# Kernel optimization log

Hardware: AMD Instinct MI355X
Metric: run time of the kernel (lower is better)

The kernel has to match this reference:

```python
import jax, jax.numpy as jnp
import numpy as np

# init kwargs (constants)
P = 1            # chamfer_distance_p
WEIGHT = 1.0
XYZ_UNIT = 0.1


def setup_inputs() -> dict:
    key = jax.random.key(0)
    k1, k2 = jax.random.split(key)
    B, N, M, D = 16, 4096, 4096, 3
    pred = jax.random.normal(k1, (B, N, D), dtype=jnp.float32)
    gt = jax.random.normal(k2, (B, M, D), dtype=jnp.float32)
    return {"pred": pred, "gt": gt}


def _chamfer(x, y, p):
    x2 = jnp.sum(x * x, axis=-1)                       # [B, N]
    y2 = jnp.sum(y * y, axis=-1)                       # [B, M]
    xy = jnp.einsum('bnd,bmd->bnm', x, y)              # [B, N, M]
    sq = jnp.maximum(x2[:, :, None] + y2[:, None, :] - 2.0 * xy, 0.0)
    dist = jnp.sqrt(sq)                                # torch.norm(x-y, dim=3)
    if p != 1:
        dist = dist ** p
    x_loss = jnp.mean(jnp.min(dist, axis=2), axis=1)   # [B]
    y_loss = jnp.mean(jnp.min(dist, axis=1), axis=1)   # [B]
    return jnp.mean(x_loss + y_loss)                   # scalar (reduce=True)


def reference(pred, gt):
    # HelperPointLoss.forward with reduce_over_batch=True, loss_name='chamfer_distance'
    loss = _chamfer(pred, gt, P)
    # info['helper_loss'] = loss (detached); info['helper_cderr'] = p=1 chamfer * xyz_unit
    cderr = _chamfer(pred, gt, 1) * XYZ_UNIT
    return (WEIGHT * loss, loss, cderr)
```

## Files before the change

### kernel.cpp

```cpp
#include <hip/hip_runtime.h>
#include <hip/hip_fp16.h>

typedef __attribute__((ext_vector_type(8)))  _Float16 half8;
typedef __attribute__((ext_vector_type(16))) float    f32x16;

#define B_   16
#define NPTS 4096

constexpr int BLK  = 256;
constexpr int WV   = 4;
constexpr int QPW  = 32;
constexpr int QPB  = WV * QPW;
constexpr int NQC  = NPTS / QPB;
constexpr int RT   = 1024;
constexpr int NR   = NPTS / RT;
constexpr int TPR  = RT / 32;
constexpr int NBLK = 2 * B_ * NQC;

__device__ __forceinline__ float min3f(float a, float b, float c) {
    return fminf(fminf(a, b), c);
}

__global__ __launch_bounds__(BLK, 4) void chamfer_mfma(
        const float* __restrict__ pred, const float* __restrict__ gt,
        float* __restrict__ accum, unsigned* __restrict__ counter,
        float* __restrict__ out) {
    const int qc  = blockIdx.x;
    const int b   = blockIdx.y;
    const int dir = blockIdx.z;
    const float* qsrc = dir ? gt   : pred;
    const float* tsrc = dir ? pred : gt;

    __shared__ uint4 sh[RT];
    __shared__ float ps[WV];

    const int tid  = threadIdx.x;
    const int lane = tid & 63;
    const int wv   = tid >> 6;
    const int m    = lane & 31;

    const float* qp = qsrc + (b * NPTS + qc * QPB + wv * QPW + m) * 3;
    __half hqx = __float2half(qp[0]);
    __half hqy = __float2half(qp[1]);
    __half hqz = __float2half(qp[2]);
    float fqx = __half2float(hqx), fqy = __half2float(hqy), fqz = __half2float(hqz);
    const float q2 = fmaf(fqx, fqx, fmaf(fqy, fqy, fqz * fqz));
    uint4 bu;
    bu.x = (unsigned)__half_as_ushort(hqx) | ((unsigned)__half_as_ushort(hqy) << 16);
    bu.y = (unsigned)__half_as_ushort(hqz) | (0x3C00u << 16);
    bu.z = 0x3C00u;
    bu.w = 0u;
    const half8 bfrag = __builtin_bit_cast(half8, bu);

    f32x16 zero;
#pragma unroll
    for (int i = 0; i < 16; ++i) zero[i] = 0.0f;

    float mn = 1e30f;

    for (int r = 0; r < NR; ++r) {
        if (r) __syncthreads();
        const float* tp = tsrc + (b * NPTS + r * RT) * 3;
#pragma unroll
        for (int k = 0; k < RT / BLK; ++k) {
            int j = k * BLK + tid;
            __half hx = __float2half(tp[3 * j + 0]);
            __half hy = __float2half(tp[3 * j + 1]);
            __half hz = __float2half(tp[3 * j + 2]);
            float fx = __half2float(hx), fy = __half2float(hy), fz = __half2float(hz);
            float g2 = fmaf(fx, fx, fmaf(fy, fy, fz * fz));
            __half ax = __float2half(-2.0f * fx);
            __half ay = __float2half(-2.0f * fy);
            __half az = __float2half(-2.0f * fz);
            __half g2hi = __float2half(g2);
            __half g2lo = __float2half(g2 - __half2float(g2hi));
            uint4 w;
            w.x = (unsigned)__half_as_ushort(ax) | ((unsigned)__half_as_ushort(ay) << 16);
            w.y = (unsigned)__half_as_ushort(az) | ((unsigned)__half_as_ushort(g2hi) << 16);
            w.z = (unsigned)__half_as_ushort(g2lo);
            w.w = 0u;
            sh[j] = w;
        }
        __syncthreads();

#pragma unroll 8
        for (int t = 0; t < TPR; ++t) {
            uint4 au = sh[t * 32 + m];
            half8 afrag = __builtin_bit_cast(half8, au);
            f32x16 d = __builtin_amdgcn_mfma_f32_32x32x16_f16(afrag, bfrag, zero, 0, 0, 0);
            float m0 = min3f(d[0],  d[1],  d[2]);
            float m1 = min3f(d[3],  d[4],  d[5]);
            float m2 = min3f(d[6],  d[7],  d[8]);
            float m3 = min3f(d[9],  d[10], d[11]);
            float m4 = min3f(d[12], d[13], d[14]);
            float n0 = min3f(m0, m1, m2);
            float n1 = min3f(m3, m4, d[15]);
            mn = min3f(mn, n0, n1);
        }
    }

    float v  = fminf(mn, __shfl_xor(mn, 32));
    float dd = fmaxf(fmaf(0.5f, v, q2), 0.0f);
    float s  = sqrtf(dd);
#pragma unroll
    for (int off = 32; off; off >>= 1) s += __shfl_xor(s, off);
    if (lane == 0) ps[wv] = 0.5f * s;
    __syncthreads();

    if (tid == 0) {
        float bs = ps[0] + ps[1] + ps[2] + ps[3];
        atomicAdd(accum, bs);
        __threadfence();
        if (atomicAdd(counter, 1u) == NBLK - 1) {
            float total = atomicAdd(accum, 0.0f);
            float loss  = total * (1.0f / (float)(B_ * NPTS));
            out[0] = loss;
            out[1] = loss;
            out[2] = 0.1f * loss;
        }
    }
}

extern "C" void kernel_launch(void* const* d_in, const int* in_sizes, int n_in,
                              void* d_out, int out_size, void* d_ws, size_t ws_size,
                              hipStream_t stream) {
    const float* pred = (const float*)d_in[0];
    const float* gt   = (const float*)d_in[1];
    float*    out     = (float*)d_out;
    float*    accum   = (float*)d_ws;
    unsigned* counter = (unsigned*)d_ws + 1;

    hipMemsetAsync(d_ws, 0, 8, stream);
    chamfer_mfma<<<dim3(NQC, B_, 2), BLK, 0, stream>>>(pred, gt, accum, counter, out);
}
```

Before: 90.40 us.

## Split target tiles across two wave groups per query set with LDS min-combine

Doubles the block to 512 threads so that two groups of four waves each process alternating target tiles for the same 128 queries. Their partial minima are then combined through shared memory before the sqrt and sum. This halves per-wave serial MFMA work and amortizes each staged LDS tile over more waves. The cost is an extra shared-memory combine, an extra barrier, and larger blocks that may limit occupancy flexibility.

```diff
diff --git a/kernel.cpp b/kernel.cpp
--- a/kernel.cpp
+++ b/kernel.cpp
@@ -7,10 +7,8 @@
 #define B_   16
 #define NPTS 4096
 
-constexpr int BLK  = 256;
-constexpr int WV   = 4;
-constexpr int QPW  = 32;
-constexpr int QPB  = WV * QPW;
+constexpr int BLK  = 512;
+constexpr int QPB  = 128;
 constexpr int NQC  = NPTS / QPB;
 constexpr int RT   = 1024;
 constexpr int NR   = NPTS / RT;
@@ -21,7 +19,7 @@
     return fminf(fminf(a, b), c);
 }
 
-__global__ __launch_bounds__(BLK, 4) void chamfer_mfma(
+__global__ __launch_bounds__(BLK, 8) void chamfer_mfma(
         const float* __restrict__ pred, const float* __restrict__ gt,
         float* __restrict__ accum, unsigned* __restrict__ counter,
         float* __restrict__ out) {
@@ -32,19 +30,24 @@
     const float* tsrc = dir ? pred : gt;
 
     __shared__ uint4 sh[RT];
-    __shared__ float ps[WV];
+    __shared__ float comb[2][QPB];
+    __shared__ float q2s[QPB];
+    __shared__ float ps[2];
 
     const int tid  = threadIdx.x;
     const int lane = tid & 63;
     const int wv   = tid >> 6;
     const int m    = lane & 31;
+    const int g    = wv & 3;
+    const int h    = wv >> 2;
 
-    const float* qp = qsrc + (b * NPTS + qc * QPB + wv * QPW + m) * 3;
+    const float* qp = qsrc + (b * NPTS + qc * QPB + g * 32 + m) * 3;
     __half hqx = __float2half(qp[0]);
     __half hqy = __float2half(qp[1]);
     __half hqz = __float2half(qp[2]);
     float fqx = __half2float(hqx), fqy = __half2float(hqy), fqz = __half2float(hqz);
     const float q2 = fmaf(fqx, fqx, fmaf(fqy, fqy, fqz * fqz));
+    if (h == 0 && lane < 32) q2s[g * 32 + m] = q2;
     uint4 bu;
     bu.x = (unsigned)__half_as_ushort(hqx) | ((unsigned)__half_as_ushort(hqy) << 16);
     bu.y = (unsigned)__half_as_ushort(hqz) | (0x3C00u << 16);
@@ -84,7 +87,7 @@
         __syncthreads();
 
 #pragma unroll 8
-        for (int t = 0; t < TPR; ++t) {
+        for (int t = h; t < TPR; t += 2) {
             uint4 au = sh[t * 32 + m];
             half8 afrag = __builtin_bit_cast(half8, au);
             f32x16 d = __builtin_amdgcn_mfma_f32_32x32x16_f16(afrag, bfrag, zero, 0, 0, 0);
@@ -99,17 +102,25 @@
         }
     }
 
-    float v  = fminf(mn, __shfl_xor(mn, 32));
-    float dd = fmaxf(fmaf(0.5f, v, q2), 0.0f);
-    float s  = sqrtf(dd);
+    float v = fminf(mn, __shfl_xor(mn, 32));
+    comb[h][g * 32 + m] = v;
+    __syncthreads();
+
+    float s = 0.0f;
+    if (tid < QPB) {
+        float vv = fminf(comb[0][tid], comb[1][tid]);
+        float dd = fmaxf(fmaf(0.5f, vv, q2s[tid]), 0.0f);
+        s = sqrtf(dd);
+    }
+    if (wv < 2) {
 #pragma unroll
-    for (int off = 32; off; off >>= 1) s += __shfl_xor(s, off);
-    if (lane == 0) ps[wv] = 0.5f * s;
+        for (int off = 32; off; off >>= 1) s += __shfl_xor(s, off);
+        if (lane == 0) ps[wv] = s;
+    }
     __syncthreads();
 
     if (tid == 0) {
-        float bs = ps[0] + ps[1] + ps[2] + ps[3];
-        atomicAdd(accum, bs);
+        atomicAdd(accum, ps[0] + ps[1]);
         __threadfence();
         if (atomicAdd(counter, 1u) == NBLK - 1) {
             float total = atomicAdd(accum, 0.0f);
```

After: 92.98 us. 1.03x slower.
